# Kernel optimization log

Measured on AMD Instinct MI355X. Metric: run time of the kernel, lower is better.

Reference implementation:

```python
import jax, jax.numpy as jnp
import numpy as np

EPS = 1e-5  # BatchNorm eps (eval mode, running_mean=0, running_var=1)


def conv1x1(x, w, b=None):
    # x: [B,C,J,T], w: [O,C] -> [B,O,J,T]
    y = jnp.einsum('oc,bcjs->bojs', w, x)
    return y if b is None else y + b[None, :, None, None]


def bn2d(x, g, b):
    s = g * (1.0 + EPS) ** -0.5
    return x * s[None, :, None, None] + b[None, :, None, None]


def norm_data(x, g, b):
    # BatchNorm1d over flattened (C*J) channels, eval mode with 0/1 stats
    bs, c, J, T = x.shape
    s = (g * (1.0 + EPS) ** -0.5).reshape(1, c, J, 1)
    return x * s + b.reshape(1, c, J, 1)


def embed(x, w1, b1, w2, b2):
    return jax.nn.relu(conv1x1(jax.nn.relu(conv1x1(x, w1, b1)), w2, b2))


def gcn_spa(x1, g, w, w1, w1b, bng, bnb):
    # g: [B,T,J,J], x1: [B,C,J,T]; permute->matmul->permute fused via einsum
    agg = jnp.einsum('bsjk,bcks->bcjs', g, x1)
    y = conv1x1(agg, w) + conv1x1(x1, w1, w1b)
    return jax.nn.relu(bn2d(y, bng, bnb))


def reference(x, spa, jbn_g, jbn_b, jw1, jb1, jw2, jb2, dbn_g, dbn_b, dw1, db1, dw2, db2,
              sw1, sb1, sw2, sb2, g1w, g1b, g2w, g2b,
              w1a, w1b_, w1bb, bn1g, bn1b, w2a, w2b_, w2bb, bn2g, bn2b,
              w3a, w3b_, w3bb, bn3g, bn3b):
    bs, c, J, T = x.shape
    dif = jnp.concatenate(
        [jnp.zeros((bs, c, J, 1), x.dtype), x[:, :, :, 1:] - x[:, :, :, :-1]], axis=-1)
    pos = embed(norm_data(x, jbn_g, jbn_b), jw1, jb1, jw2, jb2)
    spa1 = jnp.broadcast_to(embed(spa, sw1, sb1, sw2, sb2), (bs, sw2.shape[0], J, T))
    dife = embed(norm_data(dif, dbn_g, dbn_b), dw1, db1, dw2, db2)
    inp = jnp.concatenate([pos + dife, spa1], axis=1)  # [B, dim//2, J, T]
    # compute_g_spa: attention-like adjacency per frame
    q = conv1x1(inp, g1w, g1b)  # [B, dim, J, T]
    k = conv1x1(inp, g2w, g2b)
    scores = jnp.einsum('bcjs,bcks->bsjk', q, k)  # [B,T,J,J]
    g = jax.nn.softmax(scores, axis=-1)
    # GCNBig: three gcn_spa layers 128->128->256->256
    h = gcn_spa(inp, g, w1a, w1b_, w1bb, bn1g, bn1b)
    h = gcn_spa(h, g, w2a, w2b_, w2bb, bn2g, bn2b)
    h = gcn_spa(h, g, w3a, w3b_, w3bb, bn3g, bn3b)
    # AdaptiveMaxPool2d((1, seg)) with step==seg: max over joints only
    return jnp.max(h, axis=2, keepdims=True)  # [B, dim, 1, T]


def setup_inputs() -> dict:
    key = jax.random.key(0)
    bs, J, T, dim = 32, 25, 256, 256
    d4 = dim // 4  # 64
    ks = iter(jax.random.split(key, 64))
    def w(shape, s=0.05):
        return jax.random.normal(next(ks), shape, jnp.float32) * s
    inp = {}
    inp['x'] = jax.random.normal(next(ks), (bs, 3, J, T), jnp.float32)
    inp['spa'] = jnp.eye(J, dtype=jnp.float32).reshape(1, J, J, 1)
    # joint_embed
    inp['jbn_g'] = jnp.ones((3 * J,), jnp.float32); inp['jbn_b'] = w((3 * J,), 0.01)
    inp['jw1'] = w((64, 3)); inp['jb1'] = w((64,), 0.01)
    inp['jw2'] = w((d4, 64)); inp['jb2'] = w((d4,), 0.01)
    # dif_embed
    inp['dbn_g'] = jnp.ones((3 * J,), jnp.float32); inp['dbn_b'] = w((3 * J,), 0.01)
    inp['dw1'] = w((64, 3)); inp['db1'] = w((64,), 0.01)
    inp['dw2'] = w((d4, 64)); inp['db2'] = w((d4,), 0.01)
    # spa_embed (no norm)
    inp['sw1'] = w((64, J)); inp['sb1'] = w((64,), 0.01)
    inp['sw2'] = w((d4, 64)); inp['sb2'] = w((d4,), 0.01)
    # compute_g_spa: dim//2 -> dim
    inp['g1w'] = w((dim, dim // 2)); inp['g1b'] = w((dim,), 0.01)
    inp['g2w'] = w((dim, dim // 2)); inp['g2b'] = w((dim,), 0.01)
    # gcn1: 128->128
    inp['w1a'] = w((128, 128)); inp['w1b_'] = w((128, 128)); inp['w1bb'] = w((128,), 0.01)
    inp['bn1g'] = jnp.ones((128,), jnp.float32); inp['bn1b'] = w((128,), 0.01)
    # gcn2: 128->256
    inp['w2a'] = w((256, 128)); inp['w2b_'] = w((256, 128)); inp['w2bb'] = w((256,), 0.01)
    inp['bn2g'] = jnp.ones((256,), jnp.float32); inp['bn2b'] = w((256,), 0.01)
    # gcn3: 256->256
    inp['w3a'] = w((256, 256)); inp['w3b_'] = w((256, 256)); inp['w3bb'] = w((256,), 0.01)
    inp['bn3g'] = jnp.ones((256,), jnp.float32); inp['bn3b'] = w((256,), 0.01)
    return inp
```

## Files before the change

kernel.cpp:

```cpp
#include <hip/hip_runtime.h>

typedef unsigned short u16;
typedef unsigned int   u32;

#define NJ 25
#define RSC 0.99999500003750f

#define OFF_SPA1 0
#define OFF_P    2048
#define OFF_MC   16384
#define OFF_WT   32768
#define OFF_W2E  262144

#define P_JW1 0
#define P_JB1 192
#define P_JW2 256
#define P_JB2 4352
#define P_DW1 4416
#define P_DB1 4608
#define P_DW2 4672
#define P_DB2 8768
#define P_NJS 8832
#define P_NJB 8907
#define P_NDS 8982
#define P_NDB 9057
#define P_W1BB 9132
#define P_BN1S 9260
#define P_BN1B 9388
#define P_W2BB 9516
#define P_BN2S 9772
#define P_BN2B 10028
#define P_W3BB 10284
#define P_BN3S 10540
#define P_BN3B 10796
#define P_UVEC 11264
#define P_VVEC 11392
#define P_C0   11520

#define O_XF   3400
#define AUX    6800
#define A_HPH  (AUX+0)
#define A_HPL  (AUX+1800)
#define A_HDH  (AUX+3600)
#define A_HDL  (AUX+5400)
#define A_PN   (AUX+7200)
#define A_DN   (AUX+7352)
#define A_TTH  (AUX+0)
#define A_TTL  (AUX+3400)
#define A_SS   (AUX+6800)
#define A_AROW (AUX+8450)
#define A_BROW (AUX+8500)
#define A_CF   6600
#define O_G    20000
#define O_U    22000
#define ARENA  24048

typedef __attribute__((ext_vector_type(8))) short bf8;
typedef __attribute__((ext_vector_type(4))) float f4;

__device__ __forceinline__ float b2f(u16 v){
  union { u32 u; float f; } x; x.u = ((u32)v) << 16; return x.f;
}
__device__ __forceinline__ u16 f2b(float f){
  union { float f; u32 u; } x; x.f = f;
  u32 u = x.u;
  return (u16)((u + 0x7FFFu + ((u >> 16) & 1u)) >> 16);
}
__device__ __forceinline__ bool det_f32(const void* jbg){
  return ((const u16*)jbg)[0] != 0x3F80;
}
__device__ __forceinline__ float ldin(const void* p, int i, bool f32){
  if (f32) return ((const float*)p)[i];
  return b2f(((const u16*)p)[i]);
}
__device__ __forceinline__ int div25i(int e){ return (int)(((unsigned)e * 5243u) >> 17); }

__global__ void prep_all(
  const void* jw1,const void* jb1,const void* jw2,const void* jb2,
  const void* dw1,const void* db1,const void* dw2,const void* db2,
  const void* jbg,const void* jbb,const void* dbg,const void* dbb,
  const void* w1bb,const void* bn1g,const void* bn1b,
  const void* w2bb,const void* bn2g,const void* bn2b,
  const void* w3bb,const void* bn3g,const void* bn3b,
  const void* w1a,const void* w1b,const void* w2a,const void* w2b,
  const void* w3a,const void* w3b,
  const void* g1w,const void* g1b,const void* g2w,const void* g2b,
  const void* spa,const void* sw1,const void* sb1,const void* sw2,const void* sb2,
  float* W){
  __shared__ float h[64*NJ];
  bool f32 = det_f32(jbg);
  int b = blockIdx.x, tid = threadIdx.x;
  float* P = W + OFF_P;

  if (b < 44){
    int i = b*256 + tid;
    const void* s; int off; float sc = 1.f;
    if      (i < 192)  { s=jw1;  off=0; }
    else if (i < 256)  { s=jb1;  off=192; }
    else if (i < 4352) { s=jw2;  off=256; }
    else if (i < 4416) { s=jb2;  off=4352; }
    else if (i < 4608) { s=dw1;  off=4416; }
    else if (i < 4672) { s=db1;  off=4608; }
    else if (i < 8768) { s=dw2;  off=4672; }
    else if (i < 8832) { s=db2;  off=8768; }
    else if (i < 8907) { s=jbg;  off=8832; sc=RSC; }
    else if (i < 8982) { s=jbb;  off=8907; }
    else if (i < 9057) { s=dbg;  off=8982; sc=RSC; }
    else if (i < 9132) { s=dbb;  off=9057; }
    else if (i < 9260) { s=w1bb; off=9132; }
    else if (i < 9388) { s=bn1g; off=9260; sc=RSC; }
    else if (i < 9516) { s=bn1b; off=9388; }
    else if (i < 9772) { s=w2bb; off=9516; }
    else if (i < 10028){ s=bn2g; off=9772; sc=RSC; }
    else if (i < 10284){ s=bn2b; off=10028; }
    else if (i < 10540){ s=w3bb; off=10284; }
    else if (i < 10796){ s=bn3g; off=10540; sc=RSC; }
    else if (i < 11052){ s=bn3b; off=10796; }
    else return;
    P[i] = ldin(s, i - off, f32) * sc;
  } else if (b < 940){
    int i = (b-44)*256 + tid;
    u16* WTb = (u16*)(W + OFF_WT);
    const void* src; int base;
    if      (i < 16384) { src=w1a; base=0; }
    else if (i < 32768) { src=w1b; base=16384; }
    else if (i < 65536) { src=w2a; base=32768; }
    else if (i < 98304) { src=w2b; base=65536; }
    else if (i < 163840){ src=w3a; base=98304; }
    else                { src=w3b; base=163840; }
    WTb[i] = f2b(ldin(src, i - base, f32));
  } else if (b < 1005){
    int bid = b - 940;
    u16* Mhi = (u16*)(W + OFF_MC);
    if (bid < 64){
      int idx = bid*256 + tid;
      int c = idx >> 7, c2 = idx & 127;
      float s = 0.f;
      #pragma unroll 4
      for (int o = 0; o < 256; o++)
        s += ldin(g1w, o*128+c, f32) * ldin(g2w, o*128+c2, f32);
      u16 hh = f2b(s);
      Mhi[c*128+c2] = hh;
      Mhi[16384 + c*128+c2] = f2b(s - b2f(hh));
    } else {
      if (tid < 128){
        float s = 0.f;
        #pragma unroll 4
        for (int o = 0; o < 256; o++) s += ldin(g2w, o*128+tid, f32) * ldin(g1b, o, f32);
        P[P_UVEC+tid] = s;
        if (tid == 0){
          float c = 0.f;
          for (int o = 0; o < 256; o++) c += ldin(g1b, o, f32) * ldin(g2b, o, f32);
          P[P_C0] = c;
        }
      } else {
        int c2 = tid - 128;
        float s = 0.f;
        #pragma unroll 4
        for (int o = 0; o < 256; o++) s += ldin(g1w, o*128+c2, f32) * ldin(g2b, o, f32);
        P[P_VVEC+c2] = s;
      }
    }
  } else if (b == 1005){
    float* S1 = W + OFF_SPA1;
    for (int e = tid; e < 1600; e += 256){
      int o = div25i(e), j = e - o*25;
      float acc = ldin(sb1, o, f32);
      for (int c = 0; c < 25; c++) acc += ldin(sw1, o*25+c, f32) * ldin(spa, c*25+j, f32);
      h[o*25+j] = fmaxf(acc, 0.f);
    }
    __syncthreads();
    for (int e = tid; e < 1600; e += 256){
      int o2 = div25i(e), j = e - o2*25;
      float acc = ldin(sb2, o2, f32);
      for (int o = 0; o < 64; o++) acc += ldin(sw2, o2*64+o, f32) * h[o*25+j];
      S1[o2*25+j] = fmaxf(acc, 0.f);
    }
  } else {
    int i = (b-1006)*256 + tid;
    u16* W2E = (u16*)(W + OFF_W2E);
    int p = i >> 13, r = i & 8191, hl = r >> 12, e = r & 4095;
    const void* src = p ? dw2 : jw2;
    float v = ldin(src, e, f32);
    u16 hi = f2b(v);
    W2E[i] = hl ? f2b(v - b2f(hi)) : hi;
  }
}

template<int CIN, int COUT, int FINAL, int SYNCH>
__device__ __forceinline__ void gcn_layer2(const u16* WTb, int baseA, int baseB,
    short* SH, int hinOff, int sIn, int hinFS, int houtOff, int sOut, int houtFS,
    short* Uw, const float* P, int pBW, int pS, int pB,
    void* outv, bool f32o, int f0, int lane, int wave){
  const int m = lane & 15, q = lane >> 4;
  constexpr int KS  = CIN/32;
  constexpr int NMT = COUT/64;
  constexpr bool HOISTB = (CIN <= 128);

  bf8 B0h[2][HOISTB ? KS : 1], B1h[2][HOISTB ? KS : 1];
  if (HOISTB){
    #pragma unroll
    for (int fr = 0; fr < 2; fr++){
      #pragma unroll
      for (int ks = 0; ks < KS; ks++){
        B0h[fr][ks] = *(const bf8*)(SH + hinOff + fr*hinFS + m*sIn + ks*32 + q*8);
        B1h[fr][ks] = *(const bf8*)(SH + hinOff + fr*hinFS + (m+16)*sIn + ks*32 + q*8);
      }
    }
  }
  bf8 g0[2], g1[2];
  #pragma unroll
  for (int fr = 0; fr < 2; fr++){
    g0[fr] = *(const bf8*)(SH + O_G + fr*1000 + m*40 + q*8);
    g1[fr] = (bf8){0,0,0,0,0,0,0,0};
    if (m < 9) g1[fr] = *(const bf8*)(SH + O_G + fr*1000 + (m+16)*40 + q*8);
  }
  if (SYNCH) __syncthreads();

  #pragma unroll
  for (int i = 0; i < NMT; i++){
    const int co0 = wave*(COUT/4) + i*16;
    const u16* wa = WTb + baseA + (co0+m)*CIN + q*8;
    const u16* wb = WTb + baseB + (co0+m)*CIN + q*8;
    bf8 wAf[KS], wBf[KS];
    #pragma unroll
    for (int ks = 0; ks < KS; ks++){
      wAf[ks] = *(const bf8*)(wa + ks*32);
      wBf[ks] = *(const bf8*)(wb + ks*32);
    }
    #pragma unroll
    for (int fr = 0; fr < 2; fr++){
      f4 U0 = (f4){0.f,0.f,0.f,0.f}, U1 = (f4){0.f,0.f,0.f,0.f};
      f4 V0 = (f4){0.f,0.f,0.f,0.f}, V1 = (f4){0.f,0.f,0.f,0.f};
      #pragma unroll
      for (int ks = 0; ks < KS; ks++){
        bf8 b0 = HOISTB ? B0h[fr][ks] : *(const bf8*)(SH + hinOff + fr*hinFS + m*sIn + ks*32 + q*8);
        bf8 b1 = HOISTB ? B1h[fr][ks] : *(const bf8*)(SH + hinOff + fr*hinFS + (m+16)*sIn + ks*32 + q*8);
        U0 = __builtin_amdgcn_mfma_f32_16x16x32_bf16(wAf[ks], b0, U0, 0, 0, 0);
        U1 = __builtin_amdgcn_mfma_f32_16x16x32_bf16(wAf[ks], b1, U1, 0, 0, 0);
        V0 = __builtin_amdgcn_mfma_f32_16x16x32_bf16(wBf[ks], b0, V0, 0, 0, 0);
        V1 = __builtin_amdgcn_mfma_f32_16x16x32_bf16(wBf[ks], b1, V1, 0, 0, 0);
      }
      short* up = Uw + (q*4)*32 + m;
      #pragma unroll
      for (int r = 0; r < 4; r++){
        up[r*32]      = (short)f2b(U0[r]);
        up[r*32 + 16] = (m < 9) ? (short)f2b(U1[r]) : (short)0;
      }
      bf8 au = *(const bf8*)(Uw + m*32 + q*8);
      f4 Y0 = __builtin_amdgcn_mfma_f32_16x16x32_bf16(au, g0[fr], V0, 0, 0, 0);
      f4 Y1 = __builtin_amdgcn_mfma_f32_16x16x32_bf16(au, g1[fr], V1, 0, 0, 0);
      const int cob = co0 + q*4;
      if (!FINAL){
        short* Hout = SH + houtOff + fr*houtFS;
        u16 o0[4], o1[4];
        #pragma unroll
        for (int r = 0; r < 4; r++){
          float bw = P[pBW+cob+r], s = P[pS+cob+r], bb = P[pB+cob+r];
          o0[r] = f2b(fmaxf(s*(Y0[r]+bw)+bb, 0.f));
          o1[r] = f2b(fmaxf(s*(Y1[r]+bw)+bb, 0.f));
        }
        *(uint2*)(Hout + m*sOut + cob) =
            make_uint2((u32)o0[0] | ((u32)o0[1]<<16), (u32)o0[2] | ((u32)o0[3]<<16));
        if (m < 9)
          *(uint2*)(Hout + (m+16)*sOut + cob) =
              make_uint2((u32)o1[0] | ((u32)o1[1]<<16), (u32)o1[2] | ((u32)o1[3]<<16));
      } else {
        float mx[4];
        #pragma unroll
        for (int r = 0; r < 4; r++){
          float bw = P[pBW+cob+r], s = P[pS+cob+r], bb = P[pB+cob+r];
          float y0 = fmaxf(s*(Y0[r]+bw)+bb, 0.f);
          float y1 = (m < 9) ? fmaxf(s*(Y1[r]+bw)+bb, 0.f) : 0.f;
          mx[r] = fmaxf(y0, y1);
        }
        #pragma unroll
        for (int msk = 1; msk < 16; msk <<= 1){
          #pragma unroll
          for (int r = 0; r < 4; r++) mx[r] = fmaxf(mx[r], __shfl_xor(mx[r], msk, 64));
        }
        if (m == 0){
          int g = f0 + fr;
          int b = g >> 8, t = g & 255;
          #pragma unroll
          for (int r = 0; r < 4; r++){
            size_t oi = ((size_t)b*256 + cob + r)*256 + t;
            if (f32o) ((float*)outv)[oi] = mx[r];
            else      ((u16*)outv)[oi]   = f2b(mx[r]);
          }
        }
      }
    }
  }
}

__global__ __launch_bounds__(256,3) void gcn_fused(void* outv, const void* Xin, const void* jbg, float* W){
  bool f32i = det_f32(jbg);
  __shared__ __align__(16) short SH[ARENA];
  const float* P  = W + OFF_P;
  const float* S1 = W + OFF_SPA1;
  const u16* Mhi  = (const u16*)(W + OFF_MC);
  const u16* Mlo  = Mhi + 16384;
  const u16* WTb  = (const u16*)(W + OFF_WT);
  const u16* W2E  = (const u16*)(W + OFF_W2E);
  int tid = threadIdx.x;
  int lane = tid & 63, wave = tid >> 6;
  int m = lane & 15, q = lane >> 4;
  int f0 = blockIdx.x*2;

  float* pnL = (float*)(SH + A_PN);
  float* dnL = (float*)(SH + A_DN);
  float* Ss  = (float*)(SH + A_SS);
  float* arowL = (float*)(SH + A_AROW);
  float* browL = (float*)(SH + A_BROW);
  short* Uw  = SH + O_U + wave*512;

  for (int fr = 0; fr < 2; fr++){
    int g = f0 + fr, bb_ = g >> 8, t = g & 255;
    if (tid < 75){
      int c = div25i(tid), j = tid - c*25;
      int base = ((bb_*3+c)*25 + j)*256 + t;
      float v  = ldin(Xin, base, f32i);
      float vp = (t > 0) ? ldin(Xin, base-1, f32i) : v;
      pnL[c*25+j] = v*P[P_NJS+c*25+j] + P[P_NJB+c*25+j];
      dnL[c*25+j] = (v-vp)*P[P_NDS+c*25+j] + P[P_NDB+c*25+j];
    }
    __syncthreads();

    for (int i = tid; i < 3200; i += 256){
      int o = i & 63, jp = i >> 6;
      int p = div25i(jp), j = jp - p*25;
      int wb = p ? P_DW1 : P_JW1, bo = p ? P_DB1 : P_JB1;
      const float* nd = p ? dnL : pnL;
      float h = fmaxf(P[wb+o*3]*nd[j] + P[wb+o*3+1]*nd[25+j] + P[wb+o*3+2]*nd[50+j] + P[bo+o], 0.f);
      u16 hi = f2b(h);
      u16 lo = f2b(h - b2f(hi));
      short* dh = SH + (p ? A_HDH : A_HPH);
      short* dl = SH + (p ? A_HDL : A_HPL);
      dh[j*72+o] = (short)hi;
      dl[j*72+o] = (short)lo;
    }
    __syncthreads();

    {
      short* Xf = SH + fr*O_XF;
      int co0 = wave*16;
      bf8 aW[2][4];
      #pragma unroll
      for (int ks = 0; ks < 2; ks++){
        aW[ks][0] = *(const bf8*)(W2E +         (co0+m)*64 + ks*32 + q*8);
        aW[ks][1] = *(const bf8*)(W2E + 4096  + (co0+m)*64 + ks*32 + q*8);
        aW[ks][2] = *(const bf8*)(W2E + 8192  + (co0+m)*64 + ks*32 + q*8);
        aW[ks][3] = *(const bf8*)(W2E + 12288 + (co0+m)*64 + ks*32 + q*8);
      }
      f4 P0={0,0,0,0}, P1={0,0,0,0}, D0={0,0,0,0}, D1={0,0,0,0};
      #pragma unroll
      for (int ks = 0; ks < 2; ks++){
        bf8 bh0 = *(const bf8*)(SH + A_HPH + m*72      + ks*32 + q*8);
        bf8 bh1 = *(const bf8*)(SH + A_HPH + (m+16)*72 + ks*32 + q*8);
        bf8 bl0 = *(const bf8*)(SH + A_HPL + m*72      + ks*32 + q*8);
        bf8 bl1 = *(const bf8*)(SH + A_HPL + (m+16)*72 + ks*32 + q*8);
        bf8 ch0 = *(const bf8*)(SH + A_HDH + m*72      + ks*32 + q*8);
        bf8 ch1 = *(const bf8*)(SH + A_HDH + (m+16)*72 + ks*32 + q*8);
        bf8 cl0 = *(const bf8*)(SH + A_HDL + m*72      + ks*32 + q*8);
        bf8 cl1 = *(const bf8*)(SH + A_HDL + (m+16)*72 + ks*32 + q*8);
        P0 = __builtin_amdgcn_mfma_f32_16x16x32_bf16(aW[ks][0], bh0, P0, 0, 0, 0);
        P0 = __builtin_amdgcn_mfma_f32_16x16x32_bf16(aW[ks][0], bl0, P0, 0, 0, 0);
        P0 = __builtin_amdgcn_mfma_f32_16x16x32_bf16(aW[ks][1], bh0, P0, 0, 0, 0);
        P1 = __builtin_amdgcn_mfma_f32_16x16x32_bf16(aW[ks][0], bh1, P1, 0, 0, 0);
        P1 = __builtin_amdgcn_mfma_f32_16x16x32_bf16(aW[ks][0], bl1, P1, 0, 0, 0);
        P1 = __builtin_amdgcn_mfma_f32_16x16x32_bf16(aW[ks][1], bh1, P1, 0, 0, 0);
        D0 = __builtin_amdgcn_mfma_f32_16x16x32_bf16(aW[ks][2], ch0, D0, 0, 0, 0);
        D0 = __builtin_amdgcn_mfma_f32_16x16x32_bf16(aW[ks][2], cl0, D0, 0, 0, 0);
        D0 = __builtin_amdgcn_mfma_f32_16x16x32_bf16(aW[ks][3], ch0, D0, 0, 0, 0);
        D1 = __builtin_amdgcn_mfma_f32_16x16x32_bf16(aW[ks][2], ch1, D1, 0, 0, 0);
        D1 = __builtin_amdgcn_mfma_f32_16x16x32_bf16(aW[ks][2], cl1, D1, 0, 0, 0);
        D1 = __builtin_amdgcn_mfma_f32_16x16x32_bf16(aW[ks][3], ch1, D1, 0, 0, 0);
      }
      int cob = co0 + q*4;
      u16 o0[4], o1[4];
      #pragma unroll
      for (int r = 0; r < 4; r++){
        float bP = P[P_JB2+cob+r], bD = P[P_DB2+cob+r];
        o0[r] = f2b(fmaxf(P0[r]+bP, 0.f) + fmaxf(D0[r]+bD, 0.f));
        o1[r] = f2b(fmaxf(P1[r]+bP, 0.f) + fmaxf(D1[r]+bD, 0.f));
      }
      *(uint2*)(Xf + m*136 + cob) =
          make_uint2((u32)o0[0] | ((u32)o0[1]<<16), (u32)o0[2] | ((u32)o0[3]<<16));
      if (m < 9)
        *(uint2*)(Xf + (m+16)*136 + cob) =
            make_uint2((u32)o1[0] | ((u32)o1[1]<<16), (u32)o1[2] | ((u32)o1[3]<<16));
      for (int e = tid; e < 1600; e += 256){
        int o2 = div25i(e), j = e - o2*25;
        Xf[j*136 + 64 + o2] = (short)f2b(S1[o2*25 + j]);
      }
    }
    __syncthreads();
  }

  for (int fr = 0; fr < 2; fr++){
    const short* Xf = SH + fr*O_XF;
    {
      bf8 xb0[4], xb1[4];
      #pragma unroll
      for (int ks = 0; ks < 4; ks++){
        xb0[ks] = *(const bf8*)(Xf + m*136 + ks*32 + q*8);
        xb1[ks] = *(const bf8*)(Xf + (m+16)*136 + ks*32 + q*8);
      }
      #pragma unroll
      for (int i = 0; i < 2; i++){
        int co0 = wave*32 + i*16;
        const u16* mh = Mhi + (co0+m)*128 + q*8;
        const u16* ml = Mlo + (co0+m)*128 + q*8;
        bf8 mhf[4], mlf[4];
        #pragma unroll
        for (int ks = 0; ks < 4; ks++){
          mhf[ks] = *(const bf8*)(mh + ks*32);
          mlf[ks] = *(const bf8*)(ml + ks*32);
        }
        f4 t0 = {0.f,0.f,0.f,0.f}, t1 = {0.f,0.f,0.f,0.f};
        #pragma unroll
        for (int ks = 0; ks < 4; ks++){
          t0 = __builtin_amdgcn_mfma_f32_16x16x32_bf16(mlf[ks], xb0[ks], t0, 0, 0, 0);
          t0 = __builtin_amdgcn_mfma_f32_16x16x32_bf16(mhf[ks], xb0[ks], t0, 0, 0, 0);
          t1 = __builtin_amdgcn_mfma_f32_16x16x32_bf16(mlf[ks], xb1[ks], t1, 0, 0, 0);
          t1 = __builtin_amdgcn_mfma_f32_16x16x32_bf16(mhf[ks], xb1[ks], t1, 0, 0, 0);
        }
        #pragma unroll
        for (int r = 0; r < 4; r++){
          int c = co0 + q*4 + r;
          u16 h0 = f2b(t0[r]);
          SH[A_TTH + m*136 + c] = (short)h0;
          SH[A_TTL + m*136 + c] = (short)f2b(t0[r] - b2f(h0));
          if (m < 9){
            u16 h1 = f2b(t1[r]);
            SH[A_TTH + (m+16)*136 + c] = (short)h1;
            SH[A_TTL + (m+16)*136 + c] = (short)f2b(t1[r] - b2f(h1));
          }
        }
      }
    }
    if (tid < 25 || (tid >= 64 && tid < 89)){
      int j = (tid < 25) ? tid : (tid - 64);
      int pb = (tid < 25) ? P_VVEC : P_UVEC;
      float s = 0.f;
      const short* xr = Xf + j*136;
      #pragma unroll
      for (int c8 = 0; c8 < 16; c8++){
        bf8 xv = *(const bf8*)(xr + c8*8);
        #pragma unroll
        for (int e = 0; e < 8; e++) s += P[pb + c8*8 + e] * b2f((u16)xv[e]);
      }
      if (tid < 25) arowL[j] = s; else browL[j] = s;
    }
    __syncthreads();

    {
      int j0 = (wave >> 1)*16, k0 = (wave & 1)*16;
      f4 sa = {0.f,0.f,0.f,0.f};
      const short* ar = Xf + (j0+m)*136 + q*8;
      const short* bh = SH + A_TTH + (k0+m)*136 + q*8;
      const short* bl = SH + A_TTL + (k0+m)*136 + q*8;
      #pragma unroll
      for (int ks = 0; ks < 4; ks++){
        bf8 a = *(const bf8*)(ar + ks*32);
        sa = __builtin_amdgcn_mfma_f32_16x16x32_bf16(a, *(const bf8*)(bl + ks*32), sa, 0, 0, 0);
        sa = __builtin_amdgcn_mfma_f32_16x16x32_bf16(a, *(const bf8*)(bh + ks*32), sa, 0, 0, 0);
      }
      float bk = browL[k0+m] + P[P_C0];
      #pragma unroll
      for (int r = 0; r < 4; r++){
        int j = j0 + q*4 + r;
        if (j < 25) Ss[j*33 + k0 + m] = sa[r] + arowL[j] + bk;
      }
    }
    __syncthreads();

    if (tid < 25){
      short* Gf = SH + O_G + fr*1000;
      int j = tid;
      float ev[NJ]; float mx = -1e30f;
      #pragma unroll
      for (int k = 0; k < NJ; k++){ ev[k] = Ss[j*33+k]; mx = fmaxf(mx, ev[k]); }
      float s = 0.f;
      #pragma unroll
      for (int k = 0; k < NJ; k++){ ev[k] = __expf(ev[k]-mx); s += ev[k]; }
      float inv = 1.f/s;
      #pragma unroll
      for (int k = 0; k < NJ; k++) Gf[j*40+k] = (short)f2b(ev[k]*inv);
      #pragma unroll
      for (int k = NJ; k < 32; k++) Gf[j*40+k] = 0;
    }
    __syncthreads();
  }

  gcn_layer2<128,128,0,1>(WTb, 0,     16384,  SH, 0,   136, O_XF, 0,   136, O_XF,
                          Uw, P, P_W1BB, P_BN1S, P_BN1B, nullptr, false, f0, lane, wave);
  __syncthreads();
  gcn_layer2<128,256,0,0>(WTb, 32768, 65536,  SH, 0,   136, O_XF, AUX, 264, A_CF,
                          Uw, P, P_W2BB, P_BN2S, P_BN2B, nullptr, false, f0, lane, wave);
  __syncthreads();
  gcn_layer2<256,256,1,0>(WTb, 98304, 163840, SH, AUX, 264, A_CF, 0,   0,   0,
                          Uw, P, P_W3BB, P_BN3S, P_BN3B, outv, f32i, f0, lane, wave);
}

extern "C" void kernel_launch(void* const* d_in, const int* in_sizes, int n_in,
                              void* d_out, int out_size, void* d_ws, size_t ws_size,
                              hipStream_t stream){
  (void)in_sizes; (void)n_in; (void)out_size; (void)ws_size;
  const void* x    = d_in[0];
  const void* spa  = d_in[1];
  const void* jbg  = d_in[2];
  const void* jbb  = d_in[3];
  const void* jw1  = d_in[4];
  const void* jb1  = d_in[5];
  const void* jw2  = d_in[6];
  const void* jb2  = d_in[7];
  const void* dbg  = d_in[8];
  const void* dbb  = d_in[9];
  const void* dw1  = d_in[10];
  const void* db1  = d_in[11];
  const void* dw2  = d_in[12];
  const void* db2  = d_in[13];
  const void* sw1  = d_in[14];
  const void* sb1  = d_in[15];
  const void* sw2  = d_in[16];
  const void* sb2  = d_in[17];
  const void* g1w  = d_in[18];
  const void* g1b  = d_in[19];
  const void* g2w  = d_in[20];
  const void* g2b  = d_in[21];
  const void* w1a  = d_in[22];
  const void* w1b  = d_in[23];
  const void* w1bb = d_in[24];
  const void* bn1g = d_in[25];
  const void* bn1b = d_in[26];
  const void* w2a  = d_in[27];
  const void* w2b  = d_in[28];
  const void* w2bb = d_in[29];
  const void* bn2g = d_in[30];
  const void* bn2b = d_in[31];
  const void* w3a  = d_in[32];
  const void* w3b  = d_in[33];
  const void* w3bb = d_in[34];
  const void* bn3g = d_in[35];
  const void* bn3b = d_in[36];

  float* W = (float*)d_ws;

  prep_all<<<1070,256,0,stream>>>(
      jw1,jb1,jw2,jb2,dw1,db1,dw2,db2,
      jbg,jbb,dbg,dbb,
      w1bb,bn1g,bn1b,w2bb,bn2g,bn2b,w3bb,bn3g,bn3b,
      w1a,w1b,w2a,w2b,w3a,w3b,
      g1w,g1b,g2w,g2b,
      spa,sw1,sb1,sw2,sb2,
      W);
  gcn_fused<<<4096,256,0,stream>>>(d_out, x, jbg, W);
}
```

Measured before the change: 581.9 us.

## Process both frames concurrently in embed stage and interleave GCN frame MFMAs

The embed stage now handles both frames at once, with each pair of waves owning one frame, instead of looping over frames with block-wide barriers in between. The hi/lo bf16 split of the first-layer embed activations is dropped, which removes a third of the MFMAs in the second embed conv. In the GCN layers the two frames' MFMA chains are interleaved with separate per-frame U staging buffers to give more independent work, and hoisting of B fragments into registers is now chosen per layer, switched off for layer 2. The cost is lower precision in the embed path, a larger LDS arena that may reduce occupancy, and more register pressure.

```diff
diff --git a/kernel.cpp b/kernel.cpp
--- a/kernel.cpp
+++ b/kernel.cpp
@@ -39,12 +39,7 @@
 
 #define O_XF   3400
 #define AUX    6800
-#define A_HPH  (AUX+0)
-#define A_HPL  (AUX+1800)
-#define A_HDH  (AUX+3600)
-#define A_HDL  (AUX+5400)
-#define A_PN   (AUX+7200)
-#define A_DN   (AUX+7352)
+#define A_PND  (AUX+7200)
 #define A_TTH  (AUX+0)
 #define A_TTL  (AUX+3400)
 #define A_SS   (AUX+6800)
@@ -53,7 +48,7 @@
 #define A_CF   6600
 #define O_G    20000
 #define O_U    22000
-#define ARENA  24048
+#define ARENA  26096
 
 typedef __attribute__((ext_vector_type(8))) short bf8;
 typedef __attribute__((ext_vector_type(4))) float f4;
@@ -187,7 +182,7 @@
   }
 }
 
-template<int CIN, int COUT, int FINAL, int SYNCH>
+template<int CIN, int COUT, int FINAL, int SYNCH, int HOIST>
 __device__ __forceinline__ void gcn_layer2(const u16* WTb, int baseA, int baseB,
     short* SH, int hinOff, int sIn, int hinFS, int houtOff, int sOut, int houtFS,
     short* Uw, const float* P, int pBW, int pS, int pB,
@@ -195,16 +190,15 @@
   const int m = lane & 15, q = lane >> 4;
   constexpr int KS  = CIN/32;
   constexpr int NMT = COUT/64;
-  constexpr bool HOISTB = (CIN <= 128);
-
-  bf8 B0h[2][HOISTB ? KS : 1], B1h[2][HOISTB ? KS : 1];
-  if (HOISTB){
+
+  bf8 B0h[HOIST ? 2*KS : 1], B1h[HOIST ? 2*KS : 1];
+  if (HOIST){
     #pragma unroll
     for (int fr = 0; fr < 2; fr++){
       #pragma unroll
       for (int ks = 0; ks < KS; ks++){
-        B0h[fr][ks] = *(const bf8*)(SH + hinOff + fr*hinFS + m*sIn + ks*32 + q*8);
-        B1h[fr][ks] = *(const bf8*)(SH + hinOff + fr*hinFS + (m+16)*sIn + ks*32 + q*8);
+        B0h[fr*KS+ks] = *(const bf8*)(SH + hinOff + fr*hinFS + m*sIn + ks*32 + q*8);
+        B1h[fr*KS+ks] = *(const bf8*)(SH + hinOff + fr*hinFS + (m+16)*sIn + ks*32 + q*8);
       }
     }
   }
@@ -228,28 +222,40 @@
       wAf[ks] = *(const bf8*)(wa + ks*32);
       wBf[ks] = *(const bf8*)(wb + ks*32);
     }
+    f4 U0[2], U1[2], V0[2], V1[2];
     #pragma unroll
     for (int fr = 0; fr < 2; fr++){
-      f4 U0 = (f4){0.f,0.f,0.f,0.f}, U1 = (f4){0.f,0.f,0.f,0.f};
-      f4 V0 = (f4){0.f,0.f,0.f,0.f}, V1 = (f4){0.f,0.f,0.f,0.f};
-      #pragma unroll
-      for (int ks = 0; ks < KS; ks++){
-        bf8 b0 = HOISTB ? B0h[fr][ks] : *(const bf8*)(SH + hinOff + fr*hinFS + m*sIn + ks*32 + q*8);
-        bf8 b1 = HOISTB ? B1h[fr][ks] : *(const bf8*)(SH + hinOff + fr*hinFS + (m+16)*sIn + ks*32 + q*8);
-        U0 = __builtin_amdgcn_mfma_f32_16x16x32_bf16(wAf[ks], b0, U0, 0, 0, 0);
-        U1 = __builtin_amdgcn_mfma_f32_16x16x32_bf16(wAf[ks], b1, U1, 0, 0, 0);
-        V0 = __builtin_amdgcn_mfma_f32_16x16x32_bf16(wBf[ks], b0, V0, 0, 0, 0);
-        V1 = __builtin_amdgcn_mfma_f32_16x16x32_bf16(wBf[ks], b1, V1, 0, 0, 0);
-      }
-      short* up = Uw + (q*4)*32 + m;
+      U0[fr] = (f4){0.f,0.f,0.f,0.f}; U1[fr] = (f4){0.f,0.f,0.f,0.f};
+      V0[fr] = (f4){0.f,0.f,0.f,0.f}; V1[fr] = (f4){0.f,0.f,0.f,0.f};
+    }
+    #pragma unroll
+    for (int ks = 0; ks < KS; ks++){
+      #pragma unroll
+      for (int fr = 0; fr < 2; fr++){
+        bf8 b0 = HOIST ? B0h[fr*KS+ks]
+                       : *(const bf8*)(SH + hinOff + fr*hinFS + m*sIn + ks*32 + q*8);
+        bf8 b1 = HOIST ? B1h[fr*KS+ks]
+                       : *(const bf8*)(SH + hinOff + fr*hinFS + (m+16)*sIn + ks*32 + q*8);
+        U0[fr] = __builtin_amdgcn_mfma_f32_16x16x32_bf16(wAf[ks], b0, U0[fr], 0, 0, 0);
+        U1[fr] = __builtin_amdgcn_mfma_f32_16x16x32_bf16(wAf[ks], b1, U1[fr], 0, 0, 0);
+        V0[fr] = __builtin_amdgcn_mfma_f32_16x16x32_bf16(wBf[ks], b0, V0[fr], 0, 0, 0);
+        V1[fr] = __builtin_amdgcn_mfma_f32_16x16x32_bf16(wBf[ks], b1, V1[fr], 0, 0, 0);
+      }
+    }
+    #pragma unroll
+    for (int fr = 0; fr < 2; fr++){
+      short* up = Uw + fr*512 + (q*4)*32 + m;
       #pragma unroll
       for (int r = 0; r < 4; r++){
-        up[r*32]      = (short)f2b(U0[r]);
-        up[r*32 + 16] = (m < 9) ? (short)f2b(U1[r]) : (short)0;
-      }
-      bf8 au = *(const bf8*)(Uw + m*32 + q*8);
-      f4 Y0 = __builtin_amdgcn_mfma_f32_16x16x32_bf16(au, g0[fr], V0, 0, 0, 0);
-      f4 Y1 = __builtin_amdgcn_mfma_f32_16x16x32_bf16(au, g1[fr], V1, 0, 0, 0);
+        up[r*32]      = (short)f2b(U0[fr][r]);
+        up[r*32 + 16] = (m < 9) ? (short)f2b(U1[fr][r]) : (short)0;
+      }
+    }
+    #pragma unroll
+    for (int fr = 0; fr < 2; fr++){
+      bf8 au = *(const bf8*)(Uw + fr*512 + m*32 + q*8);
+      f4 Y0 = __builtin_amdgcn_mfma_f32_16x16x32_bf16(au, g0[fr], V0[fr], 0, 0, 0);
+      f4 Y1 = __builtin_amdgcn_mfma_f32_16x16x32_bf16(au, g1[fr], V1[fr], 0, 0, 0);
       const int cob = co0 + q*4;
       if (!FINAL){
         short* Hout = SH + houtOff + fr*houtFS;
@@ -308,43 +314,49 @@
   int m = lane & 15, q = lane >> 4;
   int f0 = blockIdx.x*2;
 
-  float* pnL = (float*)(SH + A_PN);
-  float* dnL = (float*)(SH + A_DN);
+  float* pnd = (float*)(SH + A_PND);
   float* Ss  = (float*)(SH + A_SS);
   float* arowL = (float*)(SH + A_AROW);
   float* browL = (float*)(SH + A_BROW);
-  short* Uw  = SH + O_U + wave*512;
-
-  for (int fr = 0; fr < 2; fr++){
-    int g = f0 + fr, bb_ = g >> 8, t = g & 255;
-    if (tid < 75){
-      int c = div25i(tid), j = tid - c*25;
-      int base = ((bb_*3+c)*25 + j)*256 + t;
-      float v  = ldin(Xin, base, f32i);
-      float vp = (t > 0) ? ldin(Xin, base-1, f32i) : v;
-      pnL[c*25+j] = v*P[P_NJS+c*25+j] + P[P_NJB+c*25+j];
-      dnL[c*25+j] = (v-vp)*P[P_NDS+c*25+j] + P[P_NDB+c*25+j];
-    }
-    __syncthreads();
-
-    for (int i = tid; i < 3200; i += 256){
+  short* Uw  = SH + O_U + wave*1024;
+
+  if (tid < 150){
+    int fr2 = (tid >= 75) ? 1 : 0;
+    int l = tid - fr2*75;
+    int c = div25i(l), j = l - c*25;
+    int g = f0 + fr2, bb_ = g >> 8, t = g & 255;
+    int base = ((bb_*3+c)*25 + j)*256 + t;
+    float v  = ldin(Xin, base, f32i);
+    float vp = (t > 0) ? ldin(Xin, base-1, f32i) : v;
+    pnd[fr2*152 + c*25+j]      = v*P[P_NJS+c*25+j] + P[P_NJB+c*25+j];
+    pnd[fr2*152 + 76 + c*25+j] = (v-vp)*P[P_NDS+c*25+j] + P[P_NDB+c*25+j];
+  }
+  __syncthreads();
+
+  {
+    int fr = wave >> 1;
+    int t2 = tid & 127;
+    const float* nd0 = pnd + fr*152;
+    short* hB = SH + AUX + fr*3600;
+    for (int i = t2; i < 3200; i += 128){
       int o = i & 63, jp = i >> 6;
       int p = div25i(jp), j = jp - p*25;
       int wb = p ? P_DW1 : P_JW1, bo = p ? P_DB1 : P_JB1;
-      const float* nd = p ? dnL : pnL;
+      const float* nd = nd0 + (p ? 76 : 0);
       float h = fmaxf(P[wb+o*3]*nd[j] + P[wb+o*3+1]*nd[25+j] + P[wb+o*3+2]*nd[50+j] + P[bo+o], 0.f);
-      u16 hi = f2b(h);
-      u16 lo = f2b(h - b2f(hi));
-      short* dh = SH + (p ? A_HDH : A_HPH);
-      short* dl = SH + (p ? A_HDL : A_HPL);
-      dh[j*72+o] = (short)hi;
-      dl[j*72+o] = (short)lo;
-    }
-    __syncthreads();
-
-    {
-      short* Xf = SH + fr*O_XF;
-      int co0 = wave*16;
+      hB[p*1800 + j*72 + o] = (short)f2b(h);
+    }
+  }
+  __syncthreads();
+
+  {
+    int fr = wave >> 1, half = wave & 1;
+    short* Xf = SH + fr*O_XF;
+    const short* hP = SH + AUX + fr*3600;
+    const short* hD = hP + 1800;
+    #pragma unroll
+    for (int i = 0; i < 2; i++){
+      int co0 = half*32 + i*16;
       bf8 aW[2][4];
       #pragma unroll
       for (int ks = 0; ks < 2; ks++){
@@ -356,25 +368,17 @@
       f4 P0={0,0,0,0}, P1={0,0,0,0}, D0={0,0,0,0}, D1={0,0,0,0};
       #pragma unroll
       for (int ks = 0; ks < 2; ks++){
-        bf8 bh0 = *(const bf8*)(SH + A_HPH + m*72      + ks*32 + q*8);
-        bf8 bh1 = *(const bf8*)(SH + A_HPH + (m+16)*72 + ks*32 + q*8);
-        bf8 bl0 = *(const bf8*)(SH + A_HPL + m*72      + ks*32 + q*8);
-        bf8 bl1 = *(const bf8*)(SH + A_HPL + (m+16)*72 + ks*32 + q*8);
-        bf8 ch0 = *(const bf8*)(SH + A_HDH + m*72      + ks*32 + q*8);
-        bf8 ch1 = *(const bf8*)(SH + A_HDH + (m+16)*72 + ks*32 + q*8);
-        bf8 cl0 = *(const bf8*)(SH + A_HDL + m*72      + ks*32 + q*8);
-        bf8 cl1 = *(const bf8*)(SH + A_HDL + (m+16)*72 + ks*32 + q*8);
+        bf8 bh0 = *(const bf8*)(hP + m*72      + ks*32 + q*8);
+        bf8 bh1 = *(const bf8*)(hP + (m+16)*72 + ks*32 + q*8);
+        bf8 ch0 = *(const bf8*)(hD + m*72      + ks*32 + q*8);
+        bf8 ch1 = *(const bf8*)(hD + (m+16)*72 + ks*32 + q*8);
         P0 = __builtin_amdgcn_mfma_f32_16x16x32_bf16(aW[ks][0], bh0, P0, 0, 0, 0);
-        P0 = __builtin_amdgcn_mfma_f32_16x16x32_bf16(aW[ks][0], bl0, P0, 0, 0, 0);
         P0 = __builtin_amdgcn_mfma_f32_16x16x32_bf16(aW[ks][1], bh0, P0, 0, 0, 0);
         P1 = __builtin_amdgcn_mfma_f32_16x16x32_bf16(aW[ks][0], bh1, P1, 0, 0, 0);
-        P1 = __builtin_amdgcn_mfma_f32_16x16x32_bf16(aW[ks][0], bl1, P1, 0, 0, 0);
         P1 = __builtin_amdgcn_mfma_f32_16x16x32_bf16(aW[ks][1], bh1, P1, 0, 0, 0);
         D0 = __builtin_amdgcn_mfma_f32_16x16x32_bf16(aW[ks][2], ch0, D0, 0, 0, 0);
-        D0 = __builtin_amdgcn_mfma_f32_16x16x32_bf16(aW[ks][2], cl0, D0, 0, 0, 0);
         D0 = __builtin_amdgcn_mfma_f32_16x16x32_bf16(aW[ks][3], ch0, D0, 0, 0, 0);
         D1 = __builtin_amdgcn_mfma_f32_16x16x32_bf16(aW[ks][2], ch1, D1, 0, 0, 0);
-        D1 = __builtin_amdgcn_mfma_f32_16x16x32_bf16(aW[ks][2], cl1, D1, 0, 0, 0);
         D1 = __builtin_amdgcn_mfma_f32_16x16x32_bf16(aW[ks][3], ch1, D1, 0, 0, 0);
       }
       int cob = co0 + q*4;
@@ -390,13 +394,15 @@
       if (m < 9)
         *(uint2*)(Xf + (m+16)*136 + cob) =
             make_uint2((u32)o1[0] | ((u32)o1[1]<<16), (u32)o1[2] | ((u32)o1[3]<<16));
-      for (int e = tid; e < 1600; e += 256){
-        int o2 = div25i(e), j = e - o2*25;
-        Xf[j*136 + 64 + o2] = (short)f2b(S1[o2*25 + j]);
-      }
-    }
-    __syncthreads();
-  }
+    }
+  }
+  for (int e = tid; e < 3200; e += 256){
+    int fr = (e >= 1600) ? 1 : 0;
+    int e2 = e - fr*1600;
+    int o2 = div25i(e2), j = e2 - o2*25;
+    SH[fr*O_XF + j*136 + 64 + o2] = (short)f2b(S1[o2*25 + j]);
+  }
+  __syncthreads();
 
   for (int fr = 0; fr < 2; fr++){
     const short* Xf = SH + fr*O_XF;
@@ -494,14 +500,14 @@
     __syncthreads();
   }
 
-  gcn_layer2<128,128,0,1>(WTb, 0,     16384,  SH, 0,   136, O_XF, 0,   136, O_XF,
-                          Uw, P, P_W1BB, P_BN1S, P_BN1B, nullptr, false, f0, lane, wave);
+  gcn_layer2<128,128,0,1,1>(WTb, 0,     16384,  SH, 0,   136, O_XF, 0,   136, O_XF,
+                            Uw, P, P_W1BB, P_BN1S, P_BN1B, nullptr, false, f0, lane, wave);
   __syncthreads();
-  gcn_layer2<128,256,0,0>(WTb, 32768, 65536,  SH, 0,   136, O_XF, AUX, 264, A_CF,
-                          Uw, P, P_W2BB, P_BN2S, P_BN2B, nullptr, false, f0, lane, wave);
+  gcn_layer2<128,256,0,0,0>(WTb, 32768, 65536,  SH, 0,   136, O_XF, AUX, 264, A_CF,
+                            Uw, P, P_W2BB, P_BN2S, P_BN2B, nullptr, false, f0, lane, wave);
   __syncthreads();
-  gcn_layer2<256,256,1,0>(WTb, 98304, 163840, SH, AUX, 264, A_CF, 0,   0,   0,
-                          Uw, P, P_W3BB, P_BN3S, P_BN3B, outv, f32i, f0, lane, wave);
+  gcn_layer2<256,256,1,0,0>(WTb, 98304, 163840, SH, AUX, 264, A_CF, 0,   0,   0,
+                            Uw, P, P_W3BB, P_BN3S, P_BN3B, outv, f32i, f0, lane, wave);
 }
 
 extern "C" void kernel_launch(void* const* d_in, const int* in_sizes, int n_in,
```

Measured after the change: 555.7 us. 1.05x faster.
